# Kernel optimization log

Measured on AMD Instinct MI355X. Metric: run time of the kernel, lower is better.

Reference implementation:

```python
import jax, jax.numpy as jnp
import numpy as np

B, N_PER, E_PER = 100, 1000, 12000  # graphs, nodes/graph, edges/graph
N, E = B * N_PER, B * E_PER
K = int(np.ceil(0.8 * N_PER))  # TopKPooling ratio=0.8 -> 800 kept nodes/graph


def setup_inputs() -> dict:
    key = jax.random.key(0)
    ks = jax.random.split(key, 16)
    g = jnp.repeat(jnp.arange(B, dtype=jnp.int64), E_PER)
    src = g * N_PER + jax.random.randint(ks[0], (E,), 0, N_PER)
    dst = g * N_PER + jax.random.randint(ks[1], (E,), 0, N_PER)
    edge_index = jnp.stack([src, dst]).astype(jnp.int64)
    edge_attr = jax.random.uniform(ks[2], (E,), dtype=jnp.float32) + 0.1  # positive edge weights
    x = jax.random.normal(ks[3], (N, 3), dtype=jnp.float32)
    batch = jnp.repeat(jnp.arange(B, dtype=jnp.int64), N_PER)
    s = 0.1
    return {
        'x': x, 'edge_index': edge_index, 'edge_attr': edge_attr, 'batch': batch,
        'conv1_w': jax.random.normal(ks[4], (3, 64), dtype=jnp.float32) * s,
        'conv1_b': jnp.zeros((64,), dtype=jnp.float32),
        'conv2_w': jax.random.normal(ks[5], (64, 64), dtype=jnp.float32) * s,
        'conv2_b': jnp.zeros((64,), dtype=jnp.float32),
        'pool_w': jax.random.normal(ks[6], (64,), dtype=jnp.float32) * s,
        'lin1_w': jax.random.normal(ks[7], (64, 64), dtype=jnp.float32) * s,
        'lin1_b': jnp.zeros((64,), dtype=jnp.float32),
        'lin2_w': jax.random.normal(ks[8], (64, 32), dtype=jnp.float32) * s,
        'lin2_b': jnp.zeros((32,), dtype=jnp.float32),
        'lin3_w': jax.random.normal(ks[9], (32, 1), dtype=jnp.float32) * s,
        'lin3_b': jnp.zeros((1,), dtype=jnp.float32),
    }


def gcn_conv(x, row, col, ew, W, b):
    # PyG GCNConv with edge_weight and implicit self-loops (weight 1):
    # deg[i] = sum_{e: col=i} ew[e] + 1;  norm_e = d^{-1/2}[row]*ew*d^{-1/2}[col]
    h = x @ W  # [N, out]
    deg = jax.ops.segment_sum(ew, col, num_segments=N) + 1.0
    dinv = jax.lax.rsqrt(deg)
    msg = (dinv[row] * ew * dinv[col])[:, None] * h[row]  # [E, out]
    out = jax.ops.segment_sum(msg, col, num_segments=N)
    out = out + (dinv * dinv)[:, None] * h  # self-loop term
    return out + b


def reference(x, edge_index, edge_attr, batch, conv1_w, conv1_b, conv2_w, conv2_b,
              pool_w, lin1_w, lin1_b, lin2_w, lin2_b, lin3_w, lin3_b):
    row, col = edge_index[0], edge_index[1]
    h = jax.nn.relu(gcn_conv(x, row, col, edge_attr, conv1_w, conv1_b))
    x1 = h.reshape(B, N_PER, 64).mean(axis=1)  # global_mean_pool (equal-size graphs)
    h = jax.nn.relu(gcn_conv(h, row, col, edge_attr, conv2_w, conv2_b))
    # TopKPooling: score = tanh(x.w / ||w||), keep top-K per graph, gate by score
    score = jnp.tanh(h @ pool_w / jnp.linalg.norm(pool_w))  # [N]
    score_bn = score.reshape(B, N_PER)
    vals, idx = jax.lax.top_k(score_bn, K)  # [B, K]
    h_bn = h.reshape(B, N_PER, 64)
    h_sel = jnp.take_along_axis(h_bn, idx[..., None], axis=1) * vals[..., None]
    x2 = h_sel.mean(axis=1)  # global_mean_pool on pooled graph
    z = x1 + x2
    z = jax.nn.relu(z @ lin1_w + lin1_b)
    z = jax.nn.relu(z @ lin2_w + lin2_b)  # dropout is identity in eval mode
    out = jax.nn.sigmoid(z @ lin3_w + lin3_b)[:, 0]
    return out
```

## Files before the change

### kernel.cpp

```cpp
#include <hip/hip_runtime.h>

#define B_G   100
#define N_PER 1000
#define E_PER 12000
#define NTOT  (B_G * N_PER)
#define ETOT  (B_G * E_PER)
#define KSEL  800
#define EPT   12

typedef __attribute__((ext_vector_type(8))) short short8;
typedef __attribute__((ext_vector_type(4))) float float4_;

__device__ __forceinline__ unsigned short f2bf(float f) {
    unsigned u = __float_as_uint(f);
    u += 0x7fffu + ((u >> 16) & 1u);
    return (unsigned short)(u >> 16);
}
__device__ __forceinline__ float bf2f(unsigned short h) {
    return __uint_as_float(((unsigned)h) << 16);
}

__global__ __launch_bounds__(1024) void k_all(
    const int* __restrict__ ei, const float* __restrict__ ew,
    const float* __restrict__ x,
    const float* __restrict__ w1, const float* __restrict__ b1,
    const float* __restrict__ w2, const float* __restrict__ b2,
    const float* __restrict__ pw,
    const float* __restrict__ l1w, const float* __restrict__ l1b,
    const float* __restrict__ l2w, const float* __restrict__ l2b,
    const float* __restrict__ l3w, const float* __restrict__ l3b,
    int2* __restrict__ csr, float* __restrict__ out) {
    __shared__ __align__(16) unsigned char smem[152832];
    unsigned short* h1s = (unsigned short*)smem;
    int*   ends = (int*)(smem + 128000);
    float* dl   = (float*)(smem + 132096);
    float* x1b  = (float*)(smem + 136192);
    unsigned char* uA = smem + 136448;

    int b = blockIdx.x, tid = threadIdx.x;
    int wid = tid >> 6, lane = tid & 63;
    int gbase = b * N_PER, ebase = b * E_PER;

    int esrc[EPT], edst[EPT]; float eww[EPT];
    int ne = (tid < (E_PER - (EPT - 1) * 1024)) ? EPT : EPT - 1;
#pragma unroll
    for (int i = 0; i < EPT; i++) {
        if (i < ne) {
            int e = tid + i * 1024;
            esrc[i] = ei[ebase + e] - gbase;
            edst[i] = ei[ETOT + ebase + e] - gbase;
            eww[i]  = ew[ebase + e];
        }
    }
    float* wsum = (float*)uA;
    int*   posc = (int*)(uA + 4096);
    ends[tid] = 0;
    wsum[tid] = 0.f;
    __syncthreads();
#pragma unroll
    for (int i = 0; i < EPT; i++)
        if (i < ne) {
            atomicAdd(&ends[edst[i]], 1);
            atomicAdd(&wsum[edst[i]], eww[i]);
        }
    __syncthreads();
    int v = ends[tid];
    int sc = v;
#pragma unroll
    for (int m = 1; m < 64; m <<= 1) {
        int t = __shfl_up(sc, m);
        if (lane >= m) sc += t;
    }
    int* wpart = (int*)x1b;
    if (lane == 63) wpart[wid] = sc;
    __syncthreads();
    if (tid < 16) {
        int s2 = wpart[tid];
#pragma unroll
        for (int m = 1; m < 16; m <<= 1) {
            int t = __shfl_up(s2, m);
            if (tid >= m) s2 += t;
        }
        wpart[tid] = s2;
    }
    __syncthreads();
    int incl = sc + (wid > 0 ? wpart[wid - 1] : 0);
    ends[tid] = incl;
    posc[tid] = incl - v;
    dl[tid] = rsqrtf(wsum[tid] + 1.0f);
    __syncthreads();
#pragma unroll
    for (int i = 0; i < EPT; i++)
        if (i < ne) {
            float cf = dl[esrc[i]] * eww[i] * dl[edst[i]];
            int p = atomicAdd(&posc[edst[i]], 1);
            csr[ebase + p] = make_int2(esrc[i], __float_as_int(cf));
        }
    __syncthreads();
    float* aggv = (float*)uA;
    if (tid < N_PER) {
        int s = (tid > 0) ? ends[tid - 1] : 0;
        int e = ends[tid];
        float a0 = 0.f, a1 = 0.f, a2 = 0.f;
        for (int k = s; k < e; k++) {
            int2 q = csr[ebase + k];
            float cf = __int_as_float(q.y);
            const float* xs = x + (size_t)(gbase + q.x) * 3;
            a0 += cf * xs[0]; a1 += cf * xs[1]; a2 += cf * xs[2];
        }
        float d2 = dl[tid] * dl[tid];
        const float* xn = x + (size_t)(gbase + tid) * 3;
        aggv[tid * 3 + 0] = a0 + d2 * xn[0];
        aggv[tid * 3 + 1] = a1 + d2 * xn[1];
        aggv[tid * 3 + 2] = a2 + d2 * xn[2];
    }
    __syncthreads();
    {
        float w0 = w1[lane], w1v = w1[64 + lane], w2v = w1[128 + lane], bf = b1[lane];
        float* sred = (float*)(uA + 12288);
        float px = 0.f;
        for (int node = wid; node < N_PER; node += 16) {
            float a0 = aggv[node * 3], a1 = aggv[node * 3 + 1], a2 = aggv[node * 3 + 2];
            float h = fmaxf(a0 * w0 + a1 * w1v + a2 * w2v + bf, 0.f);
            h1s[node * 64 + lane] = f2bf(h);
            px += h;
        }
        sred[wid * 64 + lane] = px;
        __syncthreads();
        if (tid < 64) {
            float t = 0.f;
            for (int r = 0; r < 16; r++) t += sred[r * 64 + tid];
            x1b[tid] = t * (1.0f / N_PER);
        }
    }
    __syncthreads();
    int kgrp = lane >> 4, nloc = lane & 15;
    short8 AfS[4][2];
#pragma unroll
    for (int ti = 0; ti < 4; ti++) {
        int t = wid + ti * 16;
        if (t >= 63) continue;
        int li = t * 16 + nloc;
        bool valid = li < N_PER;
        float acc[16];
        if (valid) {
            float d2 = dl[li] * dl[li];
            const unsigned short* row = h1s + li * 64;
            short8 r0 = *(const short8*)(row + kgrp * 8);
            short8 r1 = *(const short8*)(row + 32 + kgrp * 8);
#pragma unroll
            for (int j = 0; j < 8; j++) {
                acc[j]     = d2 * bf2f((unsigned short)r0[j]);
                acc[8 + j] = d2 * bf2f((unsigned short)r1[j]);
            }
        } else {
#pragma unroll
            for (int j = 0; j < 16; j++) acc[j] = 0.f;
        }
        int s = 0, cnt = 0;
        if (valid) {
            s = (li > 0) ? ends[li - 1] : 0;
            cnt = ends[li] - s;
        }
        int mx = cnt;
#pragma unroll
        for (int m = 1; m < 16; m <<= 1) mx = max(mx, __shfl_xor(mx, m));
        int base = ebase + s;
        for (int k = 0; k < mx; k++) {
            if (k < cnt) {
                int2 q = csr[base + k];
                float cf = __int_as_float(q.y);
                const unsigned short* row = h1s + q.x * 64;
                short8 r0 = *(const short8*)(row + kgrp * 8);
                short8 r1 = *(const short8*)(row + 32 + kgrp * 8);
#pragma unroll
                for (int j = 0; j < 8; j++) {
                    acc[j]     += cf * bf2f((unsigned short)r0[j]);
                    acc[8 + j] += cf * bf2f((unsigned short)r1[j]);
                }
            }
        }
        short8 a0, a1;
#pragma unroll
        for (int j = 0; j < 8; j++) {
            a0[j] = (short)f2bf(acc[j]);
            a1[j] = (short)f2bf(acc[8 + j]);
        }
        AfS[ti][0] = a0;
        AfS[ti][1] = a1;
    }
    __syncthreads();
    unsigned long long* keys = (unsigned long long*)uA;
    {
        short8 Bf[2][4];
#pragma unroll
        for (int kh = 0; kh < 2; ++kh)
#pragma unroll
            for (int c = 0; c < 4; ++c) {
                short8 t;
#pragma unroll
                for (int j = 0; j < 8; ++j)
                    t[j] = (short)f2bf(w2[(kh * 32 + kgrp * 8 + j) * 64 + c * 16 + nloc]);
                Bf[kh][c] = t;
            }
        float b2c[4], pwc[4];
#pragma unroll
        for (int c = 0; c < 4; ++c) {
            b2c[c] = b2[c * 16 + nloc];
            pwc[c] = pw[c * 16 + nloc];
        }
        float invn;
        {
            float p = pw[lane], pn = p * p;
#pragma unroll
            for (int m = 32; m; m >>= 1) pn += __shfl_xor(pn, m);
            invn = rsqrtf(pn);
        }
        if (tid >= N_PER) keys[tid] = 0ull;
#pragma unroll
        for (int ti = 0; ti < 4; ti++) {
            int t = wid + ti * 16;
            if (t >= 63) continue;
            float4_ accv[4];
#pragma unroll
            for (int c = 0; c < 4; ++c) accv[c] = (float4_){0.f, 0.f, 0.f, 0.f};
#pragma unroll
            for (int kh = 0; kh < 2; ++kh)
#pragma unroll
                for (int c = 0; c < 4; ++c)
                    accv[c] = __builtin_amdgcn_mfma_f32_16x16x32_bf16(AfS[ti][kh], Bf[kh][c], accv[c], 0, 0, 0);
#pragma unroll
            for (int r2 = 0; r2 < 4; ++r2) {
                int li2 = t * 16 + kgrp * 4 + r2;
                bool valid2 = li2 < N_PER;
                float sp = 0.f;
#pragma unroll
                for (int c = 0; c < 4; ++c) {
                    float hv = fmaxf(accv[c][r2] + b2c[c], 0.f);
                    sp += hv * pwc[c];
                    if (valid2) h1s[li2 * 64 + c * 16 + nloc] = f2bf(hv);
                }
#pragma unroll
                for (int m = 1; m < 16; m <<= 1) sp += __shfl_xor(sp, m);
                if (valid2 && nloc == 0) {
                    float scv = tanhf(sp * invn);
                    unsigned bits = __float_as_uint(scv);
                    unsigned u = (bits & 0x80000000u) ? ~bits : (bits | 0x80000000u);
                    keys[li2] = ((unsigned long long)u << 32) | (unsigned)(1023 - li2);
                }
            }
        }
    }
    __syncthreads();
    for (int k = 2; k <= 1024; k <<= 1) {
        for (int j = k >> 1; j > 0; j >>= 1) {
            int ixj = tid ^ j;
            if (ixj > tid) {
                unsigned long long a = keys[tid], c = keys[ixj];
                bool desc = ((tid & k) == 0);
                if (desc ? (a < c) : (a > c)) { keys[tid] = c; keys[ixj] = a; }
            }
            __syncthreads();
        }
    }
    float* red   = (float*)(uA + 8192);
    float* a1buf = (float*)(uA + 12288);
    float* a2buf = (float*)(uA + 12544);
    float* zbuf  = (float*)(uA + 12672);
    {
        int f = tid & 63, w16 = tid >> 6;
        float acc = 0.f;
        for (int r = w16; r < KSEL; r += 16) {
            unsigned long long key = keys[r];
            int idx = 1023 - (int)(key & 0xFFFFFFFFu);
            unsigned u = (unsigned)(key >> 32);
            unsigned bits = (u & 0x80000000u) ? (u & 0x7FFFFFFFu) : ~u;
            float val = __uint_as_float(bits);
            acc += val * bf2f(h1s[idx * 64 + f]);
        }
        red[tid] = acc;
    }
    __syncthreads();
    if (tid < 64) {
        float s2 = 0.f;
        for (int ww = 0; ww < 16; ww++) s2 += red[ww * 64 + tid];
        zbuf[tid] = x1b[tid] + s2 * (1.0f / KSEL);
    }
    __syncthreads();
    if (tid < 64) {
        float a = l1b[tid];
        for (int k = 0; k < 64; k++) a += zbuf[k] * l1w[k * 64 + tid];
        a1buf[tid] = fmaxf(a, 0.f);
    }
    __syncthreads();
    if (tid < 32) {
        float a = l2b[tid];
        for (int k = 0; k < 64; k++) a += a1buf[k] * l2w[k * 32 + tid];
        a2buf[tid] = fmaxf(a, 0.f);
    }
    __syncthreads();
    if (tid == 0) {
        float t = l3b[0];
        for (int k = 0; k < 32; k++) t += a2buf[k] * l3w[k];
        out[b] = 1.0f / (1.0f + expf(-t));
    }
}

extern "C" void kernel_launch(void* const* d_in, const int* in_sizes, int n_in,
                              void* d_out, int out_size, void* d_ws, size_t ws_size,
                              hipStream_t stream) {
    const float* x   = (const float*)d_in[0];
    const int*   ei  = (const int*)d_in[1];
    const float* ew  = (const float*)d_in[2];
    const float* c1w = (const float*)d_in[4];
    const float* c1b = (const float*)d_in[5];
    const float* c2w = (const float*)d_in[6];
    const float* c2b = (const float*)d_in[7];
    const float* pw  = (const float*)d_in[8];
    const float* l1w = (const float*)d_in[9];
    const float* l1b = (const float*)d_in[10];
    const float* l2w = (const float*)d_in[11];
    const float* l2b = (const float*)d_in[12];
    const float* l3w = (const float*)d_in[13];
    const float* l3b = (const float*)d_in[14];
    float* out = (float*)d_out;
    int2* csr = (int2*)d_ws;
    (void)ws_size; (void)in_sizes; (void)n_in; (void)out_size;

    k_all<<<B_G, 1024, 0, stream>>>(ei, ew, x, c1w, c1b, c2w, c2b, pw,
                                    l1w, l1b, l2w, l2b, l3w, l3b, csr, out);
}
```

Before: 191.4 us.

## Pack CSR to 32-bit, swizzle LDS feature rows, register bitonic sort, prefetch edges

Each CSR entry is packed into one 32-bit word: a 16-bit source index and a bf16 coefficient. This halves the global traffic for the edge list but lowers the precision of the normalization coefficient. The bf16 feature rows in LDS are XOR-swizzled by node index so that gathered short8 loads hit different banks. The top-k bitonic sort now holds its key in a register and uses wave shuffles for strides below 64, which removes most barriers. The gather loop also prefetches the next CSR entry.

```diff
diff --git a/kernel.cpp b/kernel.cpp
--- a/kernel.cpp
+++ b/kernel.cpp
@@ -18,6 +18,13 @@
 }
 __device__ __forceinline__ float bf2f(unsigned short h) {
     return __uint_as_float(((unsigned)h) << 16);
+}
+
+__device__ __forceinline__ void load_row_frag(
+    const unsigned char* h1s, int src, int kgrp, short8& r0, short8& r1) {
+    unsigned a0 = (unsigned)src * 128u + (((unsigned)(kgrp ^ (src & 7))) << 4);
+    r0 = *(const short8*)(h1s + a0);
+    r1 = *(const short8*)(h1s + (a0 ^ 64u));
 }
 
 __global__ __launch_bounds__(1024) void k_all(
@@ -29,9 +36,10 @@
     const float* __restrict__ l1w, const float* __restrict__ l1b,
     const float* __restrict__ l2w, const float* __restrict__ l2b,
     const float* __restrict__ l3w, const float* __restrict__ l3b,
-    int2* __restrict__ csr, float* __restrict__ out) {
+    unsigned* __restrict__ csr, float* __restrict__ out) {
     __shared__ __align__(16) unsigned char smem[152832];
-    unsigned short* h1s = (unsigned short*)smem;
+    unsigned char* h1s = smem;
+    unsigned short* h1u = (unsigned short*)smem;
     int*   ends = (int*)(smem + 128000);
     float* dl   = (float*)(smem + 132096);
     float* x1b  = (float*)(smem + 136192);
@@ -94,7 +102,7 @@
         if (i < ne) {
             float cf = dl[esrc[i]] * eww[i] * dl[edst[i]];
             int p = atomicAdd(&posc[edst[i]], 1);
-            csr[ebase + p] = make_int2(esrc[i], __float_as_int(cf));
+            csr[ebase + p] = ((unsigned)f2bf(cf) << 16) | (unsigned)esrc[i];
         }
     __syncthreads();
     float* aggv = (float*)uA;
@@ -103,9 +111,9 @@
         int e = ends[tid];
         float a0 = 0.f, a1 = 0.f, a2 = 0.f;
         for (int k = s; k < e; k++) {
-            int2 q = csr[ebase + k];
-            float cf = __int_as_float(q.y);
-            const float* xs = x + (size_t)(gbase + q.x) * 3;
+            unsigned q = csr[ebase + k];
+            float cf = __uint_as_float(q & 0xFFFF0000u);
+            const float* xs = x + (size_t)(gbase + (int)(q & 0xFFFFu)) * 3;
             a0 += cf * xs[0]; a1 += cf * xs[1]; a2 += cf * xs[2];
         }
         float d2 = dl[tid] * dl[tid];
@@ -119,10 +127,11 @@
         float w0 = w1[lane], w1v = w1[64 + lane], w2v = w1[128 + lane], bf = b1[lane];
         float* sred = (float*)(uA + 12288);
         float px = 0.f;
+        int swoff = (lane & 7);
         for (int node = wid; node < N_PER; node += 16) {
             float a0 = aggv[node * 3], a1 = aggv[node * 3 + 1], a2 = aggv[node * 3 + 2];
             float h = fmaxf(a0 * w0 + a1 * w1v + a2 * w2v + bf, 0.f);
-            h1s[node * 64 + lane] = f2bf(h);
+            h1u[node * 64 + ((((lane >> 3) ^ (node & 7))) << 3) + swoff] = f2bf(h);
             px += h;
         }
         sred[wid * 64 + lane] = px;
@@ -145,9 +154,8 @@
         float acc[16];
         if (valid) {
             float d2 = dl[li] * dl[li];
-            const unsigned short* row = h1s + li * 64;
-            short8 r0 = *(const short8*)(row + kgrp * 8);
-            short8 r1 = *(const short8*)(row + 32 + kgrp * 8);
+            short8 r0, r1;
+            load_row_frag(h1s, li, kgrp, r0, r1);
 #pragma unroll
             for (int j = 0; j < 8; j++) {
                 acc[j]     = d2 * bf2f((unsigned short)r0[j]);
@@ -166,19 +174,22 @@
 #pragma unroll
         for (int m = 1; m < 16; m <<= 1) mx = max(mx, __shfl_xor(mx, m));
         int base = ebase + s;
+        int cl = max(cnt - 1, 0);
+        unsigned q = csr[min(base, ETOT - 1)];
         for (int k = 0; k < mx; k++) {
+            unsigned qn = csr[min(base + min(k + 1, cl), ETOT - 1)];
             if (k < cnt) {
-                int2 q = csr[base + k];
-                float cf = __int_as_float(q.y);
-                const unsigned short* row = h1s + q.x * 64;
-                short8 r0 = *(const short8*)(row + kgrp * 8);
-                short8 r1 = *(const short8*)(row + 32 + kgrp * 8);
+                int src = (int)(q & 0xFFFFu);
+                float cf = __uint_as_float(q & 0xFFFF0000u);
+                short8 r0, r1;
+                load_row_frag(h1s, src, kgrp, r0, r1);
 #pragma unroll
                 for (int j = 0; j < 8; j++) {
                     acc[j]     += cf * bf2f((unsigned short)r0[j]);
                     acc[8 + j] += cf * bf2f((unsigned short)r1[j]);
                 }
             }
+            q = qn;
         }
         short8 a0, a1;
 #pragma unroll
@@ -238,7 +249,10 @@
                 for (int c = 0; c < 4; ++c) {
                     float hv = fmaxf(accv[c][r2] + b2c[c], 0.f);
                     sp += hv * pwc[c];
-                    if (valid2) h1s[li2 * 64 + c * 16 + nloc] = f2bf(hv);
+                    if (valid2) {
+                        int f = c * 16 + nloc;
+                        h1u[li2 * 64 + ((((f >> 3) ^ (li2 & 7))) << 3) + (f & 7)] = f2bf(hv);
+                    }
                 }
 #pragma unroll
                 for (int m = 1; m < 16; m <<= 1) sp += __shfl_xor(sp, m);
@@ -252,17 +266,29 @@
         }
     }
     __syncthreads();
-    for (int k = 2; k <= 1024; k <<= 1) {
-        for (int j = k >> 1; j > 0; j >>= 1) {
-            int ixj = tid ^ j;
-            if (ixj > tid) {
-                unsigned long long a = keys[tid], c = keys[ixj];
-                bool desc = ((tid & k) == 0);
-                if (desc ? (a < c) : (a > c)) { keys[tid] = c; keys[ixj] = a; }
-            }
-            __syncthreads();
-        }
-    }
+    {
+        unsigned long long key = keys[tid];
+        for (int k = 2; k <= 1024; k <<= 1) {
+            for (int j = k >> 1; j > 0; j >>= 1) {
+                bool desc = (tid & k) == 0;
+                unsigned long long p;
+                if (j >= 64) {
+                    keys[tid] = key;
+                    __syncthreads();
+                    p = keys[tid ^ j];
+                    __syncthreads();
+                } else {
+                    p = __shfl_xor(key, j);
+                }
+                bool low = (tid & j) == 0;
+                bool sw = low ? (desc ? (key < p) : (key > p))
+                              : (desc ? (p < key) : (p > key));
+                if (sw) key = p;
+            }
+        }
+        keys[tid] = key;
+    }
+    __syncthreads();
     float* red   = (float*)(uA + 8192);
     float* a1buf = (float*)(uA + 12288);
     float* a2buf = (float*)(uA + 12544);
@@ -276,7 +302,7 @@
             unsigned u = (unsigned)(key >> 32);
             unsigned bits = (u & 0x80000000u) ? (u & 0x7FFFFFFFu) : ~u;
             float val = __uint_as_float(bits);
-            acc += val * bf2f(h1s[idx * 64 + f]);
+            acc += val * bf2f(h1u[idx * 64 + ((((f >> 3) ^ (idx & 7))) << 3) + (f & 7)]);
         }
         red[tid] = acc;
     }
@@ -324,7 +350,7 @@
     const float* l3w = (const float*)d_in[13];
     const float* l3b = (const float*)d_in[14];
     float* out = (float*)d_out;
-    int2* csr = (int2*)d_ws;
+    unsigned* csr = (unsigned*)d_ws;
     (void)ws_size; (void)in_sizes; (void)n_in; (void)out_size;
 
     k_all<<<B_G, 1024, 0, stream>>>(ei, ew, x, c1w, c1b, c2w, c2b, pw,
```

After: 191.9 us. Within noise of the previous version (+0.2%).
